# Performance work log

Hardware: AMD Instinct MI355X
Metric: run time of the kernel (lower is better)

## Reference

```python
import jax, jax.numpy as jnp
import numpy as np

B, D_IN, H1, H2, ISO, G = 256, 5000, 2048, 1024, 100000, 25000
EPS_LN = 1e-5   # torch LayerNorm default
EPS_SM = 1e-8   # clamp_min in _gene_softmax


def setup_inputs() -> dict:
    key = jax.random.key(0)
    ks = jax.random.split(key, 6)
    rn = lambda k, sh, sc: jax.random.normal(k, sh, jnp.float32) * sc
    return {
        "x": rn(ks[0], (B, D_IN), 1.0),
        "idx": jax.random.randint(ks[1], (ISO,), 0, G),  # gene index per isoform
        "W1": rn(ks[2], (D_IN, H1), 1.0 / np.sqrt(D_IN)),
        "b1": jnp.zeros((H1,), jnp.float32),
        "g1": jnp.ones((H1,), jnp.float32),
        "beta1": jnp.zeros((H1,), jnp.float32),
        "W2": rn(ks[3], (H1, H2), 1.0 / np.sqrt(H1)),
        "b2": jnp.zeros((H2,), jnp.float32),
        "g2": jnp.ones((H2,), jnp.float32),
        "beta2": jnp.zeros((H2,), jnp.float32),
        "W3": rn(ks[4], (H2, ISO), 1.0 / np.sqrt(H2)),
        "b3": jnp.zeros((ISO,), jnp.float32),
    }


def _block(x, W, b, g, beta):
    # Linear -> LayerNorm -> GELU (dropout inactive in eval mode)
    h = x @ W + b
    mu = jnp.mean(h, axis=-1, keepdims=True)
    var = jnp.var(h, axis=-1, keepdims=True)  # biased, matches torch LN
    h = (h - mu) * jax.lax.rsqrt(var + EPS_LN) * g + beta
    return jax.nn.gelu(h, approximate=False)  # torch nn.GELU default = exact erf


def reference(x, idx, W1, b1, g1, beta1, W2, b2, g2, beta2, W3, b3):
    h = _block(x, W1, b1, g1, beta1)
    h = _block(h, W2, b2, g2, beta2)
    logits = h @ W3 + b3                                      # [B, ISO]
    # grouped (per-gene) softmax with global per-row max shift, as in source
    exp_logits = jnp.exp(logits - logits.max(axis=1, keepdims=True))
    denom = jax.ops.segment_sum(exp_logits.T, idx, num_segments=G).T  # [B, G]
    norm = jnp.maximum(denom[:, idx], EPS_SM)                 # gather back to [B, ISO]
    return exp_logits / norm
```

## Files before the change

### kernel.cpp

```cpp
#include <hip/hip_runtime.h>
#include <math.h>

#define NB   256
#define DIN  5000
#define NH1  2048
#define NH2  1024
#define NISO 100000
#define NG   25000

typedef __attribute__((ext_vector_type(8))) short bf16x8;
typedef __attribute__((ext_vector_type(4))) float f32x4;

__device__ __forceinline__ unsigned short f2bf_rn(float f) {
  union { float f; unsigned u; } v; v.f = f;
  unsigned r = v.u + 0x7FFFu + ((v.u >> 16) & 1u);
  return (unsigned short)(r >> 16);
}
__device__ __forceinline__ float bf2f(unsigned short h) {
  union { unsigned u; float f; } v; v.u = ((unsigned)h) << 16;
  return v.f;
}

template<int BN>
__global__ __launch_bounds__(256) void gemm_split(
    const float* __restrict__ A, const float* __restrict__ Bg,
    float* __restrict__ C, int M, int N, int K, int KC)
{
  constexpr int BM = 64;
  constexpr int BK = 32;
  constexpr int LDT = BK + 8;
  constexpr int CT = BN / 16;
  __shared__ unsigned short Ah[BM][LDT], Al[BM][LDT];
  __shared__ unsigned short Bh[BN][LDT], Bl[BN][LDT];
  const int tid = threadIdx.x;
  const int wave = tid >> 6, lane = tid & 63;
  const int fr = lane & 15, fq = lane >> 4;
  const int n0 = blockIdx.x * BN, m0 = blockIdx.y * BM;
  const int kb0 = blockIdx.z * KC;
  const int ke = min(kb0 + KC, K);
  const int mrow = wave * 16;
  float* Cz = C + (size_t)blockIdx.z * M * N;

  f32x4 acc[CT];
#pragma unroll
  for (int i = 0; i < CT; i++) acc[i] = (f32x4){0.f, 0.f, 0.f, 0.f};

  for (int kb = kb0; kb < ke; kb += BK) {
    for (int s = tid; s < BM * 8; s += 256) {
      int m = s >> 3, kq = (s & 7) * 4;
      int gk = kb + kq;
      const float* ap = A + (size_t)(m0 + m) * K + gk;
      float4 v;
      if (gk + 3 < ke) v = *(const float4*)ap;
      else {
        v.x = (gk     < ke) ? ap[0] : 0.f;
        v.y = (gk + 1 < ke) ? ap[1] : 0.f;
        v.z = (gk + 2 < ke) ? ap[2] : 0.f;
        v.w = (gk + 3 < ke) ? ap[3] : 0.f;
      }
      unsigned short h0 = f2bf_rn(v.x), h1 = f2bf_rn(v.y),
                     h2 = f2bf_rn(v.z), h3 = f2bf_rn(v.w);
      *(ushort4*)&Ah[m][kq] = make_ushort4(h0, h1, h2, h3);
      *(ushort4*)&Al[m][kq] = make_ushort4(f2bf_rn(v.x - bf2f(h0)),
                                           f2bf_rn(v.y - bf2f(h1)),
                                           f2bf_rn(v.z - bf2f(h2)),
                                           f2bf_rn(v.w - bf2f(h3)));
    }
    for (int s = tid; s < BN * 8; s += 256) {
      int n = s % BN, k0 = (s / BN) * 4;
      unsigned short hh[4], ll[4];
#pragma unroll
      for (int j = 0; j < 4; j++) {
        int gk = kb + k0 + j;
        float v = (gk < ke) ? Bg[(size_t)gk * N + n0 + n] : 0.f;
        hh[j] = f2bf_rn(v);
        ll[j] = f2bf_rn(v - bf2f(hh[j]));
      }
      *(ushort4*)&Bh[n][k0] = make_ushort4(hh[0], hh[1], hh[2], hh[3]);
      *(ushort4*)&Bl[n][k0] = make_ushort4(ll[0], ll[1], ll[2], ll[3]);
    }
    __syncthreads();
    bf16x8 ah = *(const bf16x8*)&Ah[mrow + fr][fq * 8];
    bf16x8 al = *(const bf16x8*)&Al[mrow + fr][fq * 8];
#pragma unroll
    for (int ct = 0; ct < CT; ct++) {
      bf16x8 bh = *(const bf16x8*)&Bh[ct * 16 + fr][fq * 8];
      bf16x8 bl = *(const bf16x8*)&Bl[ct * 16 + fr][fq * 8];
      acc[ct] = __builtin_amdgcn_mfma_f32_16x16x32_bf16(ah, bh, acc[ct], 0, 0, 0);
      acc[ct] = __builtin_amdgcn_mfma_f32_16x16x32_bf16(ah, bl, acc[ct], 0, 0, 0);
      acc[ct] = __builtin_amdgcn_mfma_f32_16x16x32_bf16(al, bh, acc[ct], 0, 0, 0);
    }
    __syncthreads();
  }
#pragma unroll
  for (int ct = 0; ct < CT; ct++) {
    int c = n0 + ct * 16 + fr;
    int r0 = m0 + mrow + fq * 4;
#pragma unroll
    for (int i = 0; i < 4; i++)
      Cz[(size_t)(r0 + i) * N + c] = acc[ct][i];
  }
}

template<bool BF16OUT>
__global__ __launch_bounds__(256) void ln_gelu_sum(
    const float* __restrict__ slabs, int nslab,
    const float* __restrict__ bias, const float* __restrict__ gam,
    const float* __restrict__ beta, void* __restrict__ outp, int n)
{
  const int r = blockIdx.x;
  float vv[8];
  float s = 0.f, s2 = 0.f;
  int cnt = 0;
  for (int j = threadIdx.x; j < n; j += 256, cnt++) {
    float v = bias[j];
    for (int z = 0; z < nslab; z++)
      v += slabs[((size_t)z * NB + r) * n + j];
    vv[cnt] = v;
    s += v; s2 += v * v;
  }
#pragma unroll
  for (int o = 32; o > 0; o >>= 1) {
    s  += __shfl_down(s, o);
    s2 += __shfl_down(s2, o);
  }
  __shared__ float red[8];
  const int wave = threadIdx.x >> 6, lane = threadIdx.x & 63;
  if (lane == 0) { red[wave] = s; red[wave + 4] = s2; }
  __syncthreads();
  if (threadIdx.x == 0) {
    float ts = 0.f, t2 = 0.f;
    for (int w = 0; w < 4; w++) { ts += red[w]; t2 += red[w + 4]; }
    float mu = ts / n;
    float var = t2 / n - mu * mu;
    red[0] = mu; red[1] = rsqrtf(var + 1e-5f);
  }
  __syncthreads();
  const float mu = red[0], rs = red[1];
  cnt = 0;
  for (int j = threadIdx.x; j < n; j += 256, cnt++) {
    float v = (vv[cnt] - mu) * rs * gam[j] + beta[j];
    float g = 0.5f * v * (1.f + erff(v * 0.70710678118654752f));
    if (BF16OUT) ((unsigned short*)outp)[(size_t)r * n + j] = f2bf_rn(g);
    else         ((float*)outp)[(size_t)r * n + j] = g;
  }
}

template<int BN>
__global__ __launch_bounds__(512, 4) void gemm3_exp(
    const unsigned short* __restrict__ Ab,
    const float* __restrict__ Bg,
    const float* __restrict__ b3,
    float* __restrict__ E)
{
  constexpr int BM = 256, BK = 128, K = NH2, N = NISO;
  constexpr int LDT = BK + 8;
  constexpr int CT = BN / 16;
  constexpr int NT = K / BK;
  constexpr int BUFS = BN * LDT;
  __shared__ unsigned short Bs[2][BN][LDT];
  const int tid = threadIdx.x;
  const int wave = tid >> 6, lane = tid & 63;
  const int fr = lane & 15, fq = lane >> 4;
  const int n0 = blockIdx.x * BN;
  const int mrow = wave * 32;

  const float* bp[5];
  int woff[5];
#pragma unroll
  for (int i = 0; i < 5; i++) {
    int s = tid + i * 512;
    int n = s % BN, k4 = s / BN;
    bp[i] = Bg + (size_t)(4 * k4) * N + n0 + n;
    woff[i] = n * LDT + k4 * 4;
  }
  unsigned short* const bs0 = &Bs[0][0][0];
  float bv[5][4];

  f32x4 acc[2][CT];
#pragma unroll
  for (int r = 0; r < 2; r++)
#pragma unroll
    for (int c = 0; c < CT; c++) acc[r][c] = (f32x4){0.f, 0.f, 0.f, 0.f};

#pragma unroll
  for (int i = 0; i < 5; i++) {
    const float* p = bp[i];
    bv[i][0] = p[0]; bv[i][1] = p[N];
    bv[i][2] = p[2 * (size_t)N]; bv[i][3] = p[3 * (size_t)N];
    bp[i] += (size_t)BK * N;
  }
#pragma unroll
  for (int i = 0; i < 5; i++)
    *(ushort4*)(bs0 + woff[i]) =
        make_ushort4(f2bf_rn(bv[i][0]), f2bf_rn(bv[i][1]),
                     f2bf_rn(bv[i][2]), f2bf_rn(bv[i][3]));

  const unsigned short* arow0 = Ab + (size_t)(mrow + fr) * K + fq * 8;
  const unsigned short* arow1 = arow0 + 16 * K;

  for (int t = 0; t < NT; ++t) {
    const int cur = t & 1;
    if (t + 1 < NT) {
#pragma unroll
      for (int i = 0; i < 5; i++) {
        const float* p = bp[i];
        bv[i][0] = p[0]; bv[i][1] = p[N];
        bv[i][2] = p[2 * (size_t)N]; bv[i][3] = p[3 * (size_t)N];
        bp[i] += (size_t)BK * N;
      }
    }
    __syncthreads();
#pragma unroll
    for (int ks = 0; ks < 4; ks++) {
      bf16x8 a0 = *(const bf16x8*)(arow0 + t * BK + ks * 32);
      bf16x8 a1 = *(const bf16x8*)(arow1 + t * BK + ks * 32);
#pragma unroll
      for (int ct = 0; ct < CT; ct++) {
        bf16x8 b = *(const bf16x8*)&Bs[cur][ct * 16 + fr][ks * 32 + fq * 8];
        acc[0][ct] = __builtin_amdgcn_mfma_f32_16x16x32_bf16(a0, b, acc[0][ct], 0, 0, 0);
        acc[1][ct] = __builtin_amdgcn_mfma_f32_16x16x32_bf16(a1, b, acc[1][ct], 0, 0, 0);
      }
    }
    if (t + 1 < NT) {
      unsigned short* wb = bs0 + (cur ^ 1) * BUFS;
#pragma unroll
      for (int i = 0; i < 5; i++)
        *(ushort4*)(wb + woff[i]) =
            make_ushort4(f2bf_rn(bv[i][0]), f2bf_rn(bv[i][1]),
                         f2bf_rn(bv[i][2]), f2bf_rn(bv[i][3]));
    }
  }
#pragma unroll
  for (int ct = 0; ct < CT; ct++) {
    const int c = n0 + ct * 16 + fr;
    const float bb = b3[c];
#pragma unroll
    for (int rt = 0; rt < 2; rt++) {
      const int r0 = mrow + rt * 16 + fq * 4;
#pragma unroll
      for (int i = 0; i < 4; i++)
        E[(size_t)(r0 + i) * N + c] = expf(acc[rt][ct][i] + bb);
    }
  }
}

__global__ __launch_bounds__(1024) void softmax_fused(
    float* __restrict__ E, const int* __restrict__ idx)
{
  __shared__ float dloc[NG];
  const int r = blockIdx.x;
  float4* Er = (float4*)(E + (size_t)r * NISO);
  const int4* I4 = (const int4*)idx;
  for (int j = threadIdx.x; j < NG; j += 1024) dloc[j] = 0.f;
  __syncthreads();
  for (int q = threadIdx.x; q < NISO / 4; q += 1024) {
    float4 v = Er[q]; int4 g = I4[q];
    atomicAdd(&dloc[g.x], v.x);
    atomicAdd(&dloc[g.y], v.y);
    atomicAdd(&dloc[g.z], v.z);
    atomicAdd(&dloc[g.w], v.w);
  }
  __syncthreads();
  for (int q = threadIdx.x; q < NISO / 4; q += 1024) {
    float4 v = Er[q]; int4 g = I4[q];
    v.x /= fmaxf(dloc[g.x], 1e-8f);
    v.y /= fmaxf(dloc[g.y], 1e-8f);
    v.z /= fmaxf(dloc[g.z], 1e-8f);
    v.w /= fmaxf(dloc[g.w], 1e-8f);
    Er[q] = v;
  }
}

extern "C" void kernel_launch(void* const* d_in, const int* in_sizes, int n_in,
                              void* d_out, int out_size, void* d_ws, size_t ws_size,
                              hipStream_t stream) {
  const float* x   = (const float*)d_in[0];
  const int*   idx = (const int*)  d_in[1];
  const float* W1  = (const float*)d_in[2];
  const float* b1  = (const float*)d_in[3];
  const float* g1  = (const float*)d_in[4];
  const float* be1 = (const float*)d_in[5];
  const float* W2  = (const float*)d_in[6];
  const float* b2  = (const float*)d_in[7];
  const float* g2  = (const float*)d_in[8];
  const float* be2 = (const float*)d_in[9];
  const float* W3  = (const float*)d_in[10];
  const float* b3  = (const float*)d_in[11];
  float* out = (float*)d_out;

  float* ws      = (float*)d_ws;
  float* h1slab  = ws;
  float* h2slab  = h1slab + (size_t)5 * NB * NH1;
  float* h1      = h2slab + (size_t)4 * NB * NH2;
  unsigned short* h2b = (unsigned short*)(h1 + (size_t)NB * NH1);

  gemm_split<128><<<dim3(NH1 / 128, NB / 64, 5), 256, 0, stream>>>(
      x, W1, h1slab, NB, NH1, DIN, 1000);
  ln_gelu_sum<false><<<NB, 256, 0, stream>>>(h1slab, 5, b1, g1, be1, h1, NH1);

  gemm_split<128><<<dim3(NH2 / 128, NB / 64, 4), 256, 0, stream>>>(
      h1, W2, h2slab, NB, NH2, NH1, 512);
  ln_gelu_sum<true><<<NB, 256, 0, stream>>>(h2slab, 4, b2, g2, be2, h2b, NH2);

  gemm3_exp<80><<<NISO / 80, 512, 0, stream>>>(h2b, W3, b3, out);

  softmax_fused<<<NB, 1024, 0, stream>>>(out, idx);
}
```

Baseline: 1.029 ms.

## Deepen W3 prefetch to two stages, batch loads in split GEMM, raise split-K

gemm3_exp now keeps two register buffers of W3 tiles so global loads run two K-steps ahead of the MFMA work, and it raises wave priority around the MFMA section. The split-K GEMM now issues all A and B global loads for a K-tile before any conversion, which gives more memory-level parallelism. Split-K factors for the first two GEMMs are doubled to launch more blocks, at the cost of larger partial-sum slabs and more reduction work in ln_gelu_sum. The extra register buffers could raise VGPR pressure under launch_bounds(512,4).

```diff
diff --git a/kernel.cpp b/kernel.cpp
--- a/kernel.cpp
+++ b/kernel.cpp
@@ -30,6 +30,8 @@
   constexpr int BK = 32;
   constexpr int LDT = BK + 8;
   constexpr int CT = BN / 16;
+  constexpr int AT = BM * 8 / 256;
+  constexpr int BT = BN * 8 / 256;
   __shared__ unsigned short Ah[BM][LDT], Al[BM][LDT];
   __shared__ unsigned short Bh[BN][LDT], Bl[BN][LDT];
   const int tid = threadIdx.x;
@@ -46,7 +48,10 @@
   for (int i = 0; i < CT; i++) acc[i] = (f32x4){0.f, 0.f, 0.f, 0.f};
 
   for (int kb = kb0; kb < ke; kb += BK) {
-    for (int s = tid; s < BM * 8; s += 256) {
+    float4 av[AT];
+#pragma unroll
+    for (int u = 0; u < AT; u++) {
+      int s = tid + u * 256;
       int m = s >> 3, kq = (s & 7) * 4;
       int gk = kb + kq;
       const float* ap = A + (size_t)(m0 + m) * K + gk;
@@ -58,6 +63,24 @@
         v.z = (gk + 2 < ke) ? ap[2] : 0.f;
         v.w = (gk + 3 < ke) ? ap[3] : 0.f;
       }
+      av[u] = v;
+    }
+    float bw[BT][4];
+#pragma unroll
+    for (int u = 0; u < BT; u++) {
+      int s = tid + u * 256;
+      int n = s % BN, k0 = (s / BN) * 4;
+#pragma unroll
+      for (int j = 0; j < 4; j++) {
+        int gk = kb + k0 + j;
+        bw[u][j] = (gk < ke) ? Bg[(size_t)gk * N + n0 + n] : 0.f;
+      }
+    }
+#pragma unroll
+    for (int u = 0; u < AT; u++) {
+      int s = tid + u * 256;
+      int m = s >> 3, kq = (s & 7) * 4;
+      float4 v = av[u];
       unsigned short h0 = f2bf_rn(v.x), h1 = f2bf_rn(v.y),
                      h2 = f2bf_rn(v.z), h3 = f2bf_rn(v.w);
       *(ushort4*)&Ah[m][kq] = make_ushort4(h0, h1, h2, h3);
@@ -66,15 +89,15 @@
                                            f2bf_rn(v.z - bf2f(h2)),
                                            f2bf_rn(v.w - bf2f(h3)));
     }
-    for (int s = tid; s < BN * 8; s += 256) {
+#pragma unroll
+    for (int u = 0; u < BT; u++) {
+      int s = tid + u * 256;
       int n = s % BN, k0 = (s / BN) * 4;
       unsigned short hh[4], ll[4];
 #pragma unroll
       for (int j = 0; j < 4; j++) {
-        int gk = kb + k0 + j;
-        float v = (gk < ke) ? Bg[(size_t)gk * N + n0 + n] : 0.f;
-        hh[j] = f2bf_rn(v);
-        ll[j] = f2bf_rn(v - bf2f(hh[j]));
+        hh[j] = f2bf_rn(bw[u][j]);
+        ll[j] = f2bf_rn(bw[u][j] - bf2f(hh[j]));
       }
       *(ushort4*)&Bh[n][k0] = make_ushort4(hh[0], hh[1], hh[2], hh[3]);
       *(ushort4*)&Bl[n][k0] = make_ushort4(ll[0], ll[1], ll[2], ll[3]);
@@ -145,6 +168,21 @@
     else         ((float*)outp)[(size_t)r * n + j] = g;
   }
 }
+
+#define G3_LOAD(bv)                                             \
+  _Pragma("unroll")                                             \
+  for (int i = 0; i < 5; i++) {                                 \
+    const float* p = bp[i];                                     \
+    bv[i][0] = p[0]; bv[i][1] = p[N];                           \
+    bv[i][2] = p[2 * (size_t)N]; bv[i][3] = p[3 * (size_t)N];   \
+    bp[i] += (size_t)BK * N;                                    \
+  }
+#define G3_WRITE(bv, wb)                                        \
+  _Pragma("unroll")                                             \
+  for (int i = 0; i < 5; i++)                                   \
+    *(ushort4*)((wb) + woff[i]) =                               \
+        make_ushort4(f2bf_rn(bv[i][0]), f2bf_rn(bv[i][1]),      \
+                     f2bf_rn(bv[i][2]), f2bf_rn(bv[i][3]));
 
 template<int BN>
 __global__ __launch_bounds__(512, 4) void gemm3_exp(
@@ -175,7 +213,7 @@
     woff[i] = n * LDT + k4 * 4;
   }
   unsigned short* const bs0 = &Bs[0][0][0];
-  float bv[5][4];
+  float bvE[5][4], bvO[5][4];
 
   f32x4 acc[2][CT];
 #pragma unroll
@@ -183,34 +221,22 @@
 #pragma unroll
     for (int c = 0; c < CT; c++) acc[r][c] = (f32x4){0.f, 0.f, 0.f, 0.f};
 
-#pragma unroll
-  for (int i = 0; i < 5; i++) {
-    const float* p = bp[i];
-    bv[i][0] = p[0]; bv[i][1] = p[N];
-    bv[i][2] = p[2 * (size_t)N]; bv[i][3] = p[3 * (size_t)N];
-    bp[i] += (size_t)BK * N;
-  }
-#pragma unroll
-  for (int i = 0; i < 5; i++)
-    *(ushort4*)(bs0 + woff[i]) =
-        make_ushort4(f2bf_rn(bv[i][0]), f2bf_rn(bv[i][1]),
-                     f2bf_rn(bv[i][2]), f2bf_rn(bv[i][3]));
+  G3_LOAD(bvE);
+  G3_LOAD(bvO);
+  G3_WRITE(bvE, bs0);
 
   const unsigned short* arow0 = Ab + (size_t)(mrow + fr) * K + fq * 8;
   const unsigned short* arow1 = arow0 + 16 * K;
 
+#pragma unroll
   for (int t = 0; t < NT; ++t) {
     const int cur = t & 1;
-    if (t + 1 < NT) {
-#pragma unroll
-      for (int i = 0; i < 5; i++) {
-        const float* p = bp[i];
-        bv[i][0] = p[0]; bv[i][1] = p[N];
-        bv[i][2] = p[2 * (size_t)N]; bv[i][3] = p[3 * (size_t)N];
-        bp[i] += (size_t)BK * N;
-      }
+    if (t + 2 < NT) {
+      if (cur == 0) { G3_LOAD(bvE); }
+      else          { G3_LOAD(bvO); }
     }
     __syncthreads();
+    __builtin_amdgcn_s_setprio(1);
 #pragma unroll
     for (int ks = 0; ks < 4; ks++) {
       bf16x8 a0 = *(const bf16x8*)(arow0 + t * BK + ks * 32);
@@ -222,13 +248,11 @@
         acc[1][ct] = __builtin_amdgcn_mfma_f32_16x16x32_bf16(a1, b, acc[1][ct], 0, 0, 0);
       }
     }
+    __builtin_amdgcn_s_setprio(0);
     if (t + 1 < NT) {
       unsigned short* wb = bs0 + (cur ^ 1) * BUFS;
-#pragma unroll
-      for (int i = 0; i < 5; i++)
-        *(ushort4*)(wb + woff[i]) =
-            make_ushort4(f2bf_rn(bv[i][0]), f2bf_rn(bv[i][1]),
-                         f2bf_rn(bv[i][2]), f2bf_rn(bv[i][3]));
+      if (cur == 0) { G3_WRITE(bvO, wb); }
+      else          { G3_WRITE(bvE, wb); }
     }
   }
 #pragma unroll
@@ -291,17 +315,17 @@
 
   float* ws      = (float*)d_ws;
   float* h1slab  = ws;
-  float* h2slab  = h1slab + (size_t)5 * NB * NH1;
-  float* h1      = h2slab + (size_t)4 * NB * NH2;
+  float* h2slab  = h1slab + (size_t)10 * NB * NH1;
+  float* h1      = h2slab + (size_t)8 * NB * NH2;
   unsigned short* h2b = (unsigned short*)(h1 + (size_t)NB * NH1);
 
-  gemm_split<128><<<dim3(NH1 / 128, NB / 64, 5), 256, 0, stream>>>(
-      x, W1, h1slab, NB, NH1, DIN, 1000);
-  ln_gelu_sum<false><<<NB, 256, 0, stream>>>(h1slab, 5, b1, g1, be1, h1, NH1);
-
-  gemm_split<128><<<dim3(NH2 / 128, NB / 64, 4), 256, 0, stream>>>(
-      h1, W2, h2slab, NB, NH2, NH1, 512);
-  ln_gelu_sum<true><<<NB, 256, 0, stream>>>(h2slab, 4, b2, g2, be2, h2b, NH2);
+  gemm_split<128><<<dim3(NH1 / 128, NB / 64, 10), 256, 0, stream>>>(
+      x, W1, h1slab, NB, NH1, DIN, 500);
+  ln_gelu_sum<false><<<NB, 256, 0, stream>>>(h1slab, 10, b1, g1, be1, h1, NH1);
+
+  gemm_split<128><<<dim3(NH2 / 128, NB / 64, 8), 256, 0, stream>>>(
+      h1, W2, h2slab, NB, NH2, NH1, 256);
+  ln_gelu_sum<true><<<NB, 256, 0, stream>>>(h2slab, 8, b2, g2, be2, h2b, NH2);
 
   gemm3_exp<80><<<NISO / 80, 512, 0, stream>>>(h2b, W3, b3, out);
 
```

After: 911.0 us. 11.5% less time.
